# Performance work log

Hardware: AMD Instinct MI355X
Metric: run time of the kernel (lower is better)

The kernel has to match this reference:

```python
import jax, jax.numpy as jnp
import numpy as np

B, S, IN, OUT = 4, 2048, 4096, 4096

def setup_inputs() -> dict:
    key = jax.random.key(0)
    k1, k2, k3, k4 = jax.random.split(key, 4)
    input = jax.random.normal(k1, (B, S, IN), dtype=jnp.float32)
    # int8-valued weights stored as int32 (range [-128, 127])
    weight_int8 = jax.random.randint(k2, (OUT, IN), -128, 128, dtype=jnp.int32)
    scale = jax.random.uniform(k3, (OUT, 1), dtype=jnp.float32, minval=0.001, maxval=0.02)
    zero_point = jnp.zeros((OUT, 1), dtype=jnp.float32)
    bias = jax.random.normal(k4, (OUT,), dtype=jnp.float32)
    return {"input": input, "weight_int8": weight_int8, "scale": scale,
            "zero_point": zero_point, "bias": bias}

def reference(input, weight_int8, scale, zero_point, bias):
    # Dequantize: per-output-channel affine (w - zp) * s, then linear.
    w = (weight_int8.astype(input.dtype) - zero_point) * scale  # [OUT, IN]
    out = jnp.einsum('bsi,oi->bso', input, w)
    return out + bias
```

## Files before the change

kernel.cpp:

```cpp
#include <hip/hip_runtime.h>
#include <cstdint>
#include <cstddef>


#define BM 128
#define BN 128
#define BK 32

typedef __bf16 bf16x8 __attribute__((ext_vector_type(8)));
typedef float floatx4 __attribute__((ext_vector_type(4)));
typedef float float4v __attribute__((ext_vector_type(4)));
typedef int int4v __attribute__((ext_vector_type(4)));
typedef unsigned short ushort8v __attribute__((ext_vector_type(8)));
typedef unsigned short ushort4v __attribute__((ext_vector_type(4)));

#define AS1 __attribute__((address_space(1)))
#define AS3 __attribute__((address_space(3)))

__device__ __forceinline__ void load16_g2l(const void* g, void* l) {
    __builtin_amdgcn_global_load_lds((const AS1 void*)(uintptr_t)g,
                                     (AS3 void*)(uint32_t)(uintptr_t)l,
                                     16, 0, 0);
}

__device__ __forceinline__ unsigned short f2bf(float f) {
    union { float f; uint32_t u; } v; v.f = f;
    uint32_t u = v.u;
    uint32_t r = (u + 0x7fffu + ((u >> 16) & 1u)) >> 16;
    return (unsigned short)r;
}

__global__ __launch_bounds__(256) void prep(
    const float* __restrict__ a_in, unsigned short* __restrict__ a_out,
    const int* __restrict__ w, const float* __restrict__ scale,
    const float* __restrict__ zp, unsigned short* __restrict__ w_out,
    int ga_blocks) {
    const int bid = blockIdx.x;
    if (bid < ga_blocks) {
        const size_t i = ((size_t)bid * 256 + threadIdx.x) * 4;
        float4v f = *(const float4v*)(a_in + i);
        ushort4v r;
        r[0] = f2bf(f[0]); r[1] = f2bf(f[1]); r[2] = f2bf(f[2]); r[3] = f2bf(f[3]);
        *(ushort4v*)(a_out + i) = r;
    } else {
        const size_t i = ((size_t)(bid - ga_blocks) * 256 + threadIdx.x) * 4;
        const int row = (int)(i >> 12);
        const float s = scale[row];
        const float z = zp[row];
        int4v wv = *(const int4v*)(w + i);
        ushort4v o;
        o[0] = f2bf(((float)wv[0] - z) * s);
        o[1] = f2bf(((float)wv[1] - z) * s);
        o[2] = f2bf(((float)wv[2] - z) * s);
        o[3] = f2bf(((float)wv[3] - z) * s);
        *(ushort4v*)(w_out + i) = o;
    }
}

__global__ __launch_bounds__(256) void gemm_bf16_bt(
    const unsigned short* __restrict__ A,
    const unsigned short* __restrict__ B,
    const float* __restrict__ bias,
    float* __restrict__ C,
    int M, int N, int K) {
    __shared__ unsigned short lds_a[BM * BK];
    __shared__ unsigned short lds_b[BN * BK];

    const int tid = threadIdx.x;
    const int lane = tid & 63;
    const int wave = tid >> 6;

    const int n0 = blockIdx.x * BN;
    const int m0 = blockIdx.y * BM;

    const int wm = (wave >> 1) * 64;
    const int wn = (wave & 1) * 64;

    floatx4 acc[4][4];
    const floatx4 zero = {0.f, 0.f, 0.f, 0.f};
#pragma unroll
    for (int i = 0; i < 4; ++i)
#pragma unroll
        for (int j = 0; j < 4; ++j) acc[i][j] = zero;

    const int fl0 = tid, fl1 = tid + 256;
    const int row0 = fl0 >> 2, row1 = fl1 >> 2;
    const int kc0 = (((fl0 & 3) ^ ((row0 >> 1) & 3)) * 8);
    const int kc1 = (((fl1 & 3) ^ ((row1 >> 1) & 3)) * 8);

    const unsigned short* ga0 = A + (size_t)(m0 + row0) * K + kc0;
    const unsigned short* ga1 = A + (size_t)(m0 + row1) * K + kc1;
    const unsigned short* gb0 = B + (size_t)(n0 + row0) * K + kc0;
    const unsigned short* gb1 = B + (size_t)(n0 + row1) * K + kc1;

    unsigned short* la0 = &lds_a[fl0 * 8];
    unsigned short* la1 = &lds_a[fl1 * 8];
    unsigned short* lb0 = &lds_b[fl0 * 8];
    unsigned short* lb1 = &lds_b[fl1 * 8];

    const int fm = lane & 15;
    const int fq = lane >> 4;
    const int swz = fq ^ ((fm >> 1) & 3);

    const unsigned short* ra[4];
    const unsigned short* rb[4];
#pragma unroll
    for (int t = 0; t < 4; ++t) {
        const int pa = (wm + t * 16 + fm) * 4 + swz;
        const int pb = (wn + t * 16 + fm) * 4 + swz;
        ra[t] = &lds_a[pa * 8];
        rb[t] = &lds_b[pb * 8];
    }

    for (int k0 = 0; k0 < K; k0 += BK) {
        __syncthreads();
        load16_g2l(ga0 + k0, la0);
        load16_g2l(ga1 + k0, la1);
        load16_g2l(gb0 + k0, lb0);
        load16_g2l(gb1 + k0, lb1);
        __syncthreads();

        bf16x8 av[4], bv[4];
#pragma unroll
        for (int t = 0; t < 4; ++t) av[t] = *(const bf16x8*)ra[t];
#pragma unroll
        for (int t = 0; t < 4; ++t) bv[t] = *(const bf16x8*)rb[t];
#pragma unroll
        for (int i = 0; i < 4; ++i)
#pragma unroll
            for (int j = 0; j < 4; ++j)
                acc[i][j] = __builtin_amdgcn_mfma_f32_16x16x32_bf16(
                    av[i], bv[j], acc[i][j], 0, 0, 0);
    }

#pragma unroll
    for (int j = 0; j < 4; ++j) {
        const int col = n0 + wn + j * 16 + fm;
        const float bvl = bias[col];
#pragma unroll
        for (int i = 0; i < 4; ++i) {
            const int rbase = m0 + wm + i * 16 + fq * 4;
#pragma unroll
            for (int r = 0; r < 4; ++r) {
                C[(size_t)(rbase + r) * N + col] = acc[i][j][r] + bvl;
            }
        }
    }
}

__global__ __launch_bounds__(256) void fallback_naive(
    const float* __restrict__ in, const int* __restrict__ w,
    const float* __restrict__ scale, const float* __restrict__ zp,
    const float* __restrict__ bias, float* __restrict__ out,
    int M, int N, int K) {
    int idx = blockIdx.x * 256 + threadIdx.x;
    if (idx >= M * N) return;
    int m = idx / N, n = idx - m * N;
    const float s = scale[n], z = zp[n];
    const float* a = in + (size_t)m * K;
    const int* wr = w + (size_t)n * K;
    float acc = 0.f;
    for (int k = 0; k < K; ++k) acc += a[k] * ((float)wr[k] - z);
    out[idx] = acc * s + bias[n];
}

extern "C" void kernel_launch(void* const* d_in, const int* in_sizes, int n_in,
                              void* d_out, int out_size, void* d_ws, size_t ws_size,
                              hipStream_t stream) {
    constexpr int M = 4 * 2048;
    constexpr int K = 4096;
    constexpr int N = 4096;

    const float* input = (const float*)d_in[0];
    const int* w8 = (const int*)d_in[1];
    const float* scale = (const float*)d_in[2];
    const float* zp = (const float*)d_in[3];
    const float* bias = (const float*)d_in[4];
    float* out = (float*)d_out;

    const size_t need = ((size_t)M * K + (size_t)N * K) * sizeof(unsigned short);
    if (ws_size < need) {
        const int total = M * N;
        fallback_naive<<<(total + 255) / 256, 256, 0, stream>>>(
            input, w8, scale, zp, bias, out, M, N, K);
        return;
    }

    unsigned short* wsA = (unsigned short*)d_ws;
    unsigned short* wsW = wsA + (size_t)M * K;

    const int ga_blocks = (M * K) / 1024;
    const int gw_blocks = (N * K) / 1024;
    prep<<<ga_blocks + gw_blocks, 256, 0, stream>>>(
        input, wsA, w8, scale, zp, wsW, ga_blocks);

    dim3 grid(N / BN, M / BM);
    gemm_bf16_bt<<<grid, 256, 0, stream>>>(wsA, wsW, bias, out, M, N, K);
}
```

Before: 600.0 us.

## Use 256x256 tiles with 4-stage LDS pipeline, block swizzle, wider prep

The GEMM moves to 256x256 tiles with 512 threads, so each wave computes a 128x64 sub-tile. It replaces the single-buffer, two-barrier loop with a 4-stage ring of global-to-LDS buffers that prefetch three steps ahead, split-phase barriers, and MFMA priority boosts. It also remaps block IDs with an XCD-aware swizzle and makes the prep kernel handle 8 elements per thread. The aim is to hide global-load latency and raise data reuse. In exchange it uses much more LDS (128 KB) and more accumulator registers, which may cut occupancy, and it hardcodes K and the grid width.

Result: faster. 527.1 us (-12.1%).

```diff
diff --git a/kernel.cpp b/kernel.cpp
--- a/kernel.cpp
+++ b/kernel.cpp
@@ -3,16 +3,17 @@
 #include <cstddef>
 
 
-#define BM 128
-#define BN 128
+#define BM 256
+#define BN 256
 #define BK 32
+#define KDIM 4096
+#define NT (KDIM / BK)
 
 typedef __bf16 bf16x8 __attribute__((ext_vector_type(8)));
 typedef float floatx4 __attribute__((ext_vector_type(4)));
 typedef float float4v __attribute__((ext_vector_type(4)));
 typedef int int4v __attribute__((ext_vector_type(4)));
 typedef unsigned short ushort8v __attribute__((ext_vector_type(8)));
-typedef unsigned short ushort4v __attribute__((ext_vector_type(4)));
 
 #define AS1 __attribute__((address_space(1)))
 #define AS3 __attribute__((address_space(3)))
@@ -34,103 +35,157 @@
     const float* __restrict__ a_in, unsigned short* __restrict__ a_out,
     const int* __restrict__ w, const float* __restrict__ scale,
     const float* __restrict__ zp, unsigned short* __restrict__ w_out,
-    int ga_blocks) {
-    const int bid = blockIdx.x;
-    if (bid < ga_blocks) {
-        const size_t i = ((size_t)bid * 256 + threadIdx.x) * 4;
-        float4v f = *(const float4v*)(a_in + i);
-        ushort4v r;
-        r[0] = f2bf(f[0]); r[1] = f2bf(f[1]); r[2] = f2bf(f[2]); r[3] = f2bf(f[3]);
-        *(ushort4v*)(a_out + i) = r;
+    int ga_units) {
+    const long long u = (long long)blockIdx.x * 256 + threadIdx.x;
+    if (u < ga_units) {
+        const size_t i = (size_t)u * 8;
+        float4v f0 = *(const float4v*)(a_in + i);
+        float4v f1 = *(const float4v*)(a_in + i + 4);
+        ushort8v r;
+        r[0] = f2bf(f0[0]); r[1] = f2bf(f0[1]);
+        r[2] = f2bf(f0[2]); r[3] = f2bf(f0[3]);
+        r[4] = f2bf(f1[0]); r[5] = f2bf(f1[1]);
+        r[6] = f2bf(f1[2]); r[7] = f2bf(f1[3]);
+        *(ushort8v*)(a_out + i) = r;
     } else {
-        const size_t i = ((size_t)(bid - ga_blocks) * 256 + threadIdx.x) * 4;
+        const size_t i = (size_t)(u - ga_units) * 8;
         const int row = (int)(i >> 12);
         const float s = scale[row];
         const float z = zp[row];
-        int4v wv = *(const int4v*)(w + i);
-        ushort4v o;
-        o[0] = f2bf(((float)wv[0] - z) * s);
-        o[1] = f2bf(((float)wv[1] - z) * s);
-        o[2] = f2bf(((float)wv[2] - z) * s);
-        o[3] = f2bf(((float)wv[3] - z) * s);
-        *(ushort4v*)(w_out + i) = o;
-    }
-}
-
-__global__ __launch_bounds__(256) void gemm_bf16_bt(
+        int4v w0 = *(const int4v*)(w + i);
+        int4v w1 = *(const int4v*)(w + i + 4);
+        ushort8v o;
+        o[0] = f2bf(((float)w0[0] - z) * s);
+        o[1] = f2bf(((float)w0[1] - z) * s);
+        o[2] = f2bf(((float)w0[2] - z) * s);
+        o[3] = f2bf(((float)w0[3] - z) * s);
+        o[4] = f2bf(((float)w1[0] - z) * s);
+        o[5] = f2bf(((float)w1[1] - z) * s);
+        o[6] = f2bf(((float)w1[2] - z) * s);
+        o[7] = f2bf(((float)w1[3] - z) * s);
+        *(ushort8v*)(w_out + i) = o;
+    }
+}
+
+__global__ __launch_bounds__(512, 2) void gemm_bf16_bt(
     const unsigned short* __restrict__ A,
-    const unsigned short* __restrict__ B,
+    const unsigned short* __restrict__ Bm,
     const float* __restrict__ bias,
     float* __restrict__ C,
     int M, int N, int K) {
-    __shared__ unsigned short lds_a[BM * BK];
-    __shared__ unsigned short lds_b[BN * BK];
+    __shared__ unsigned short lds_a[4][BM * BK];
+    __shared__ unsigned short lds_b[4][BN * BK];
 
     const int tid = threadIdx.x;
     const int lane = tid & 63;
-    const int wave = tid >> 6;
-
-    const int n0 = blockIdx.x * BN;
-    const int m0 = blockIdx.y * BM;
-
-    const int wm = (wave >> 1) * 64;
-    const int wn = (wave & 1) * 64;
-
-    floatx4 acc[4][4];
+    const int wv = tid >> 6;
+    const int wm = (wv >> 2) * 128;
+    const int wn = (wv & 3) * 64;
+
+    const int nwg = gridDim.x;
+    const int b = blockIdx.x;
+    const int swz = (b & 7) * (nwg >> 3) + (b >> 3);
+    const int bx = swz & 15;
+    const int by = swz >> 4;
+    const int n0 = bx * BN;
+    const int m0 = by * BM;
+
+    floatx4 acc[8][4];
     const floatx4 zero = {0.f, 0.f, 0.f, 0.f};
 #pragma unroll
-    for (int i = 0; i < 4; ++i)
+    for (int i = 0; i < 8; ++i)
 #pragma unroll
         for (int j = 0; j < 4; ++j) acc[i][j] = zero;
 
-    const int fl0 = tid, fl1 = tid + 256;
-    const int row0 = fl0 >> 2, row1 = fl1 >> 2;
-    const int kc0 = (((fl0 & 3) ^ ((row0 >> 1) & 3)) * 8);
-    const int kc1 = (((fl1 & 3) ^ ((row1 >> 1) & 3)) * 8);
-
-    const unsigned short* ga0 = A + (size_t)(m0 + row0) * K + kc0;
-    const unsigned short* ga1 = A + (size_t)(m0 + row1) * K + kc1;
-    const unsigned short* gb0 = B + (size_t)(n0 + row0) * K + kc0;
-    const unsigned short* gb1 = B + (size_t)(n0 + row1) * K + kc1;
-
-    unsigned short* la0 = &lds_a[fl0 * 8];
-    unsigned short* la1 = &lds_a[fl1 * 8];
-    unsigned short* lb0 = &lds_b[fl0 * 8];
-    unsigned short* lb1 = &lds_b[fl1 * 8];
+    const int fl0 = tid, fl1 = tid + 512;
+    const int r0 = fl0 >> 2, r1 = fl1 >> 2;
+    const int kc0 = ((fl0 & 3) ^ ((r0 >> 1) & 3)) * 8;
+    const int kc1 = ((fl1 & 3) ^ ((r1 >> 1) & 3)) * 8;
+    const unsigned short* gA0 = A + (size_t)(m0 + r0) * K + kc0;
+    const unsigned short* gA1 = A + (size_t)(m0 + r1) * K + kc1;
+    const unsigned short* gB0 = Bm + (size_t)(n0 + r0) * K + kc0;
+    const unsigned short* gB1 = Bm + (size_t)(n0 + r1) * K + kc1;
+    const int lo0 = fl0 * 8, lo1 = fl1 * 8;
 
     const int fm = lane & 15;
     const int fq = lane >> 4;
-    const int swz = fq ^ ((fm >> 1) & 3);
-
-    const unsigned short* ra[4];
-    const unsigned short* rb[4];
-#pragma unroll
-    for (int t = 0; t < 4; ++t) {
-        const int pa = (wm + t * 16 + fm) * 4 + swz;
-        const int pb = (wn + t * 16 + fm) * 4 + swz;
-        ra[t] = &lds_a[pa * 8];
-        rb[t] = &lds_b[pb * 8];
-    }
-
-    for (int k0 = 0; k0 < K; k0 += BK) {
-        __syncthreads();
-        load16_g2l(ga0 + k0, la0);
-        load16_g2l(ga1 + k0, la1);
-        load16_g2l(gb0 + k0, lb0);
-        load16_g2l(gb1 + k0, lb1);
-        __syncthreads();
+    const int swzf = fq ^ ((fm >> 1) & 3);
+    int pA[8], pB[4];
+#pragma unroll
+    for (int i = 0; i < 8; ++i) pA[i] = ((wm + i * 16 + fm) * 4 + swzf) * 8;
+#pragma unroll
+    for (int j = 0; j < 4; ++j) pB[j] = ((wn + j * 16 + fm) * 4 + swzf) * 8;
+
+#pragma unroll
+    for (int tt = 0; tt < 3; ++tt) {
+        const int kk = tt * BK;
+        unsigned short* sa = lds_a[tt];
+        unsigned short* sb = lds_b[tt];
+        load16_g2l(gA0 + kk, sa + lo0);
+        load16_g2l(gA1 + kk, sa + lo1);
+        load16_g2l(gB0 + kk, sb + lo0);
+        load16_g2l(gB1 + kk, sb + lo1);
+    }
+    asm volatile("s_waitcnt vmcnt(8)" ::: "memory");
+    __builtin_amdgcn_s_barrier();
+    asm volatile("" ::: "memory");
+
+#pragma unroll 1
+    for (int t = 0; t < NT; ++t) {
+        const unsigned short* la = lds_a[t & 3];
+        const unsigned short* lb = lds_b[t & 3];
+        const bool st = (t < NT - 3);
+        const int kk = (t + 3) * BK;
+        unsigned short* sa = lds_a[(t + 3) & 3];
+        unsigned short* sb = lds_b[(t + 3) & 3];
 
         bf16x8 av[4], bv[4];
 #pragma unroll
-        for (int t = 0; t < 4; ++t) av[t] = *(const bf16x8*)ra[t];
-#pragma unroll
-        for (int t = 0; t < 4; ++t) bv[t] = *(const bf16x8*)rb[t];
+        for (int j = 0; j < 4; ++j) bv[j] = *(const bf16x8*)(lb + pB[j]);
+#pragma unroll
+        for (int i = 0; i < 4; ++i) av[i] = *(const bf16x8*)(la + pA[i]);
+        if (st) {
+            load16_g2l(gA0 + kk, sa + lo0);
+            load16_g2l(gA1 + kk, sa + lo1);
+        }
+        __builtin_amdgcn_s_barrier();
+        asm volatile("s_waitcnt lgkmcnt(0)" ::: "memory");
+        __builtin_amdgcn_s_setprio(1);
 #pragma unroll
         for (int i = 0; i < 4; ++i)
 #pragma unroll
             for (int j = 0; j < 4; ++j)
                 acc[i][j] = __builtin_amdgcn_mfma_f32_16x16x32_bf16(
                     av[i], bv[j], acc[i][j], 0, 0, 0);
+        __builtin_amdgcn_s_setprio(0);
+        __builtin_amdgcn_s_barrier();
+
+        bf16x8 av2[4];
+#pragma unroll
+        for (int i = 0; i < 4; ++i) av2[i] = *(const bf16x8*)(la + pA[i + 4]);
+        if (st) {
+            load16_g2l(gB0 + kk, sb + lo0);
+            load16_g2l(gB1 + kk, sb + lo1);
+        }
+        __builtin_amdgcn_s_barrier();
+        asm volatile("s_waitcnt lgkmcnt(0)" ::: "memory");
+        __builtin_amdgcn_s_setprio(1);
+#pragma unroll
+        for (int i = 0; i < 4; ++i)
+#pragma unroll
+            for (int j = 0; j < 4; ++j)
+                acc[i + 4][j] = __builtin_amdgcn_mfma_f32_16x16x32_bf16(
+                    av2[i], bv[j], acc[i + 4][j], 0, 0, 0);
+        __builtin_amdgcn_s_setprio(0);
+
+        if (t < NT - 3)
+            asm volatile("s_waitcnt vmcnt(8)" ::: "memory");
+        else if (t == NT - 3)
+            asm volatile("s_waitcnt vmcnt(4)" ::: "memory");
+        else if (t == NT - 2)
+            asm volatile("s_waitcnt vmcnt(0)" ::: "memory");
+        __builtin_amdgcn_s_barrier();
+        asm volatile("" ::: "memory");
     }
 
 #pragma unroll
@@ -138,7 +193,7 @@
         const int col = n0 + wn + j * 16 + fm;
         const float bvl = bias[col];
 #pragma unroll
-        for (int i = 0; i < 4; ++i) {
+        for (int i = 0; i < 8; ++i) {
             const int rbase = m0 + wm + i * 16 + fq * 4;
 #pragma unroll
             for (int r = 0; r < 4; ++r) {
@@ -189,11 +244,12 @@
     unsigned short* wsA = (unsigned short*)d_ws;
     unsigned short* wsW = wsA + (size_t)M * K;
 
-    const int ga_blocks = (M * K) / 1024;
-    const int gw_blocks = (N * K) / 1024;
-    prep<<<ga_blocks + gw_blocks, 256, 0, stream>>>(
-        input, wsA, w8, scale, zp, wsW, ga_blocks);
-
-    dim3 grid(N / BN, M / BM);
-    gemm_bf16_bt<<<grid, 256, 0, stream>>>(wsA, wsW, bias, out, M, N, K);
-}
+    const int ga_units = (M * K) / 8;
+    const int gw_units = (N * K) / 8;
+    const int prep_blocks = (ga_units + gw_units) / 256;
+    prep<<<prep_blocks, 256, 0, stream>>>(
+        input, wsA, w8, scale, zp, wsW, ga_units);
+
+    dim3 grid((N / BN) * (M / BM));
+    gemm_bf16_bt<<<grid, 512, 0, stream>>>(wsA, wsW, bias, out, M, N, K);
+}
```
